# Kernel optimization log

Hardware: AMD Instinct MI355X
Metric: run time of the kernel (lower is better)

## Reference

```python
import jax, jax.numpy as jnp
import numpy as np

KS = 5               # kernel_size per spline dimension
K3 = KS ** 3         # 125 weight matrices per SplineConv
NS = [16384, 4096, 1024, 256, 64]  # nodes per hierarchy level
DEG = 8


def spline_basis(pseudo):
    """Degree-1 open B-spline basis for 3D pseudo-coords in [0,1].
    Returns basis [E,8] and weight indices [E,8] into the K3 weights."""
    v = pseudo * (KS - 1)
    bot = jnp.minimum(jnp.floor(v), KS - 2)
    frac = v - bot                                  # [E,3]
    bot = bot.astype(jnp.int32)
    bits = jnp.array([[(s >> d) & 1 for d in range(3)] for s in range(8)], jnp.int32)  # [8,3]
    f = frac[:, None, :]                            # [E,1,3]
    basis = jnp.prod(jnp.where(bits[None] == 1, f, 1.0 - f), axis=-1)   # [E,8]
    strides = jnp.array([1, KS, KS * KS], jnp.int32)
    widx = jnp.sum((bot[:, None, :] + bits[None]) * strides, axis=-1)   # [E,8]
    return basis, widx


def spline_conv(x, src, dst, basis, widx, W, root, bias, n):
    """out_j = (1/deg_j) * sum_{i->j} sum_s B_s(u_ij) x_i W_{k(s)} + x_j root + bias.
    Accumulate basis-weighted source features into per-(node, weight-index)
    buckets, then one dense einsum with the 125 kernel weights."""
    in_c = x.shape[1]
    contrib = basis[..., None] * x[src][:, None, :]          # [E,8,in]
    flat = (dst[:, None] * K3 + widx).reshape(-1)            # [E*8]
    acc = jnp.zeros((n * K3, in_c), x.dtype).at[flat].add(contrib.reshape(-1, in_c))
    out = jnp.einsum('nki,kio->no', acc.reshape(n, K3, in_c), W)
    deg = jnp.zeros((n,), x.dtype).at[dst].add(1.0)
    return out / jnp.maximum(deg, 1.0)[:, None] + x @ root + bias


def setup_inputs() -> dict:
    rng = np.random.default_rng(0)
    inp = {}
    inp['x'] = jnp.asarray(rng.standard_normal((NS[0], 1)), jnp.float32)
    for l in range(4):
        e = NS[l] * DEG
        inp[f'src{l}'] = jnp.asarray(rng.integers(0, NS[l], e), jnp.int32)
        inp[f'dst{l}'] = jnp.asarray(rng.integers(0, NS[l], e), jnp.int32)
        inp[f'pseudo{l}'] = jnp.asarray(rng.random((e, 3)), jnp.float32)
        cl = np.arange(NS[l]) % NS[l + 1]  # guarantees every voxel cluster non-empty
        rng.shuffle(cl)
        inp[f'cluster{l}'] = jnp.asarray(cl, jnp.int32)
    chans = [(1, 32), (32, 32), (32, 64), (64, 64), (64, 64), (64, 64), (64, 64), (64, 64)]
    names = ['1', '12', '2', '3', '4', '5', '6', '7']
    for nm, (ci, co) in zip(names, chans):
        inp[f'W{nm}'] = jnp.asarray(rng.standard_normal((K3, ci, co)) / np.sqrt(8.0 * ci), jnp.float32)
        inp[f'R{nm}'] = jnp.asarray(rng.standard_normal((ci, co)) / np.sqrt(ci), jnp.float32)
        inp[f'B{nm}'] = jnp.zeros((co,), jnp.float32)
    inp['fc1_w'] = jnp.asarray(rng.standard_normal((64, 64)) / 8.0, jnp.float32)
    inp['fc1_b'] = jnp.zeros((64,), jnp.float32)
    inp['fc2_w'] = jnp.asarray(rng.standard_normal((64, 10)) / 8.0, jnp.float32)
    inp['fc2_b'] = jnp.zeros((10,), jnp.float32)
    return inp


def reference(x, pseudo0, pseudo1, pseudo2, pseudo3,
              src0, dst0, src1, dst1, src2, dst2, src3, dst3,
              cluster0, cluster1, cluster2, cluster3,
              W1, R1, B1, W12, R12, B12, W2, R2, B2, W3, R3, B3,
              W4, R4, B4, W5, R5, B5, W6, R6, B6, W7, R7, B7,
              fc1_w, fc1_b, fc2_w, fc2_b):
    elu = jax.nn.elu
    # level 0
    b, wi = spline_basis(pseudo0)
    h = elu(spline_conv(x, src0, dst0, b, wi, W1, R1, B1, NS[0]))
    h = elu(spline_conv(h, src0, dst0, b, wi, W12, R12, B12, NS[0]))
    h = jax.ops.segment_max(h, cluster0, num_segments=NS[1])   # voxel max pool 1
    # level 1
    b, wi = spline_basis(pseudo1)
    h = elu(spline_conv(h, src1, dst1, b, wi, W2, R2, B2, NS[1]))
    h = elu(spline_conv(h, src1, dst1, b, wi, W3, R3, B3, NS[1]))
    h = jax.ops.segment_max(h, cluster1, num_segments=NS[2])   # voxel max pool 2
    # level 2
    b, wi = spline_basis(pseudo2)
    h = elu(spline_conv(h, src2, dst2, b, wi, W4, R4, B4, NS[2]))
    h = elu(spline_conv(h, src2, dst2, b, wi, W5, R5, B5, NS[2]))
    h = jax.ops.segment_max(h, cluster2, num_segments=NS[3])   # voxel max pool 3
    # level 3
    b, wi = spline_basis(pseudo3)
    h = elu(spline_conv(h, src3, dst3, b, wi, W6, R6, B6, NS[3]))
    h = elu(spline_conv(h, src3, dst3, b, wi, W7, R7, B7, NS[3]))
    h = jax.ops.segment_max(h, cluster3, num_segments=NS[4])   # voxel max pool 4
    # readout head (dropout is identity in eval mode)
    g = h.mean(0)[None, :]
    g = g @ fc1_w + fc1_b
    g = g @ fc2_w + fc2_b
    return jax.nn.log_softmax(g, axis=1)
```

## Files before the change

### kernel.cpp

```cpp
#include <hip/hip_runtime.h>
#include <hip/hip_bf16.h>

#define KS 5
#define K3 125

typedef __attribute__((ext_vector_type(8))) short short8;
typedef __attribute__((ext_vector_type(4))) float floatx4;

__device__ inline unsigned enc_f(float f) {
    int b = __float_as_int(f);
    return (b >= 0) ? ((unsigned)b | 0x80000000u) : ~((unsigned)b);
}

__device__ inline unsigned short f2bf(float f) {
    unsigned u = __float_as_uint(f);
    u += 0x7FFFu + ((u >> 16) & 1u);
    return (unsigned short)(u >> 16);
}
__device__ inline float bf2f(unsigned short h) {
    return __uint_as_float((unsigned)h << 16);
}
__device__ inline unsigned pack2bf(float a, float b) {
    return (unsigned)f2bf(a) | ((unsigned)f2bf(b) << 16);
}

__device__ inline void edge_basis(const float* __restrict__ pseudo, int e,
                                  float* bs, int* ks) {
    float fr[3];
    int bot[3];
#pragma unroll
    for (int d = 0; d < 3; ++d) {
        float v = pseudo[e * 3 + d] * (float)(KS - 1);
        float fl = fminf(floorf(v), (float)(KS - 2));
        fr[d] = v - fl;
        bot[d] = (int)fl;
    }
    const int strides[3] = {1, KS, KS * KS};
#pragma unroll
    for (int s = 0; s < 8; ++s) {
        float b = 1.f;
        int w = 0;
#pragma unroll
        for (int d = 0; d < 3; ++d) {
            int bit = (s >> d) & 1;
            b *= bit ? fr[d] : (1.f - fr[d]);
            w += (bot[d] + bit) * strides[d];
        }
        bs[s] = b;
        ks[s] = w;
    }
}

__device__ inline void edge_fracs(const float* __restrict__ pseudo, int e, float* bs) {
    float fr[3];
#pragma unroll
    for (int d = 0; d < 3; ++d) {
        float v = pseudo[e * 3 + d] * (float)(KS - 1);
        float fl = fminf(floorf(v), (float)(KS - 2));
        fr[d] = v - fl;
    }
#pragma unroll
    for (int s = 0; s < 8; ++s) {
        float b = 1.f;
#pragma unroll
        for (int d = 0; d < 3; ++d) b *= ((s >> d) & 1) ? fr[d] : (1.f - fr[d]);
        bs[s] = b;
    }
}

__device__ inline int edge_bucket(const float* __restrict__ pseudo, int e) {
    int kb = 0;
#pragma unroll
    for (int d = 0; d < 3; ++d) {
        float v = pseudo[e * 3 + d] * (float)(KS - 1);
        int fl = (int)fminf(floorf(v), (float)(KS - 2));
        kb += fl << (2 * d);
    }
    return kb;
}

__global__ __launch_bounds__(256) void pre1(
    const float* __restrict__ p0, const float* __restrict__ p1,
    const float* __restrict__ p2, const float* __restrict__ p3,
    const int* __restrict__ d0, const int* __restrict__ d1,
    const int* __restrict__ d2, const int* __restrict__ d3,
    const int* __restrict__ c0, const int* __restrict__ c1,
    const int* __restrict__ c2, const int* __restrict__ c3,
    const float* __restrict__ w12, const float* __restrict__ w2,
    const float* __restrict__ w3, const float* __restrict__ w4,
    const float* __restrict__ w5, const float* __restrict__ w6,
    const float* __restrict__ w7,
    int* __restrict__ hpart, int* __restrict__ degi,
    int* __restrict__ ccnt, int* __restrict__ clist,
    short* __restrict__ Wt) {
    int b = blockIdx.x;
    if (b >= 765) {
        int idx = (b - 765) * 256 + threadIdx.x;
        if (idx >= 2944000) return;
        const float* Wsrc;
        int lgP, lgI, local;
        if (idx < 128000)       { Wsrc = w12; lgP = 10; lgI = 5; local = idx; }
        else if (idx < 384000)  { Wsrc = w2;  lgP = 11; lgI = 5; local = idx - 128000; }
        else if (idx < 896000)  { Wsrc = w3;  lgP = 12; lgI = 6; local = idx - 384000; }
        else if (idx < 1408000) { Wsrc = w4;  lgP = 12; lgI = 6; local = idx - 896000; }
        else if (idx < 1920000) { Wsrc = w5;  lgP = 12; lgI = 6; local = idx - 1408000; }
        else if (idx < 2432000) { Wsrc = w6;  lgP = 12; lgI = 6; local = idx - 1920000; }
        else                    { Wsrc = w7;  lgP = 12; lgI = 6; local = idx - 2432000; }
        int IC = 1 << lgI;
        int OC = 1 << (lgP - lgI);
        int k = local >> lgP;
        int r = local & ((1 << lgP) - 1);
        int o = r >> lgI;
        int i = r & (IC - 1);
        Wt[idx] = (short)f2bf(Wsrc[(size_t)(k * IC + i) * OC + o]);
        return;
    }
    if (b >= 680) {
        int idx = (b - 680) * 256 + threadIdx.x;
        int j, cof, nof;
        const int* cl;
        if (idx < 16384)      { j = idx;         cl = c0; cof = 0;    nof = 0; }
        else if (idx < 20480) { j = idx - 16384; cl = c1; cof = 4096; nof = 16384; }
        else if (idx < 21504) { j = idx - 20480; cl = c2; cof = 5120; nof = 20480; }
        else if (idx < 21760) { j = idx - 21504; cl = c3; cof = 5376; nof = 21504; }
        else return;
        int c = cl[j];
        int slot = atomicAdd(&ccnt[cof + c], 1) & 3;
        clist[nof + c * 4 + slot] = j;
        return;
    }
    int l, lb, E, dof;
    const float* ps;
    const int* ds;
    if (b < 512)      { l = 0; lb = b;       ps = p0; ds = d0; E = 131072; dof = 0; }
    else if (b < 640) { l = 1; lb = b - 512; ps = p1; ds = d1; E = 32768;  dof = 16384; }
    else if (b < 672) { l = 2; lb = b - 640; ps = p2; ds = d2; E = 8192;   dof = 20480; }
    else              { l = 3; lb = b - 672; ps = p3; ds = d3; E = 2048;   dof = 21504; }
    __shared__ int h[64];
    int t = threadIdx.x;
    if (t < 64) h[t] = 0;
    __syncthreads();
    int e = lb * 256 + t;
    if (e < E) {
        atomicAdd(&h[edge_bucket(ps, e)], 1);
        atomicAdd(&degi[dof + ds[e]], 1);
    }
    __syncthreads();
    if (t < 64) hpart[b * 64 + t] = h[t];
}

__global__ __launch_bounds__(1024) void pre2(const int* __restrict__ hpart,
                                             int* __restrict__ bbase,
                                             int* __restrict__ tileOf,
                                             int* __restrict__ pack,
                                             const int* __restrict__ degi,
                                             int* __restrict__ off,
                                             int* __restrict__ cur) {
    int b = blockIdx.x;
    int t = threadIdx.x;
    __shared__ int ls[1024];
    __shared__ int aux[192];
    if (b < 4) {
        const int Nv[4] = {16384, 4096, 1024, 256};
        const int DOFv[4] = {0, 16384, 20480, 21504};
        const int OFFv[4] = {0, 16385, 20482, 21507};
        int l = b;
        int n = Nv[l];
        const int* d = degi + DOFv[l];
        int* o = off + OFFv[l];
        int* c = cur + DOFv[l];
        int per = (n + 1023) >> 10;
        int beg = t * per;
        int end = (beg + per < n) ? beg + per : n;
        int s = 0;
        for (int j = beg; j < end; ++j) s += d[j];
        ls[t] = s;
        __syncthreads();
        for (int dd = 1; dd < 1024; dd <<= 1) {
            int v = (t >= dd) ? ls[t - dd] : 0;
            __syncthreads();
            ls[t] += v;
            __syncthreads();
        }
        int base = (t == 0) ? 0 : ls[t - 1];
        for (int j = beg; j < end; ++j) {
            o[j] = base;
            c[j] = base;
            base += d[j];
        }
        if (t == 1023) o[n] = ls[1023];
    } else {
        const int TBv[4] = {0, 2112, 2688, 2880};
        const int MTv[4] = {2112, 576, 192, 96};
        const int HBv[4] = {0, 512, 640, 672};
        const int NBv[4] = {512, 128, 32, 8};
        int l = b - 4;
        int tileBase = TBv[l];
        int hb = HBv[l], nb = NBv[l];
        int bucket = t & 63, seg = t >> 6;
        int rps = (nb + 15) >> 4;
        int r0 = seg * rps;
        int r1 = r0 + rps;
        if (r1 > nb) r1 = nb;
        int ssum = 0;
        for (int lb = r0; lb < r1; ++lb) ssum += hpart[(hb + lb) * 64 + bucket];
        ls[seg * 64 + bucket] = ssum;
        __syncthreads();
        int pre = 0;
        for (int s2 = 0; s2 < seg; ++s2) pre += ls[s2 * 64 + bucket];
        if (seg == 15) aux[bucket] = pre + ssum;
        __syncthreads();
        if (t < 64) aux[64 + t] = (aux[t] + 63) >> 6;
        __syncthreads();
        for (int d = 1; d < 64; d <<= 1) {
            int v = 0;
            if (t < 64 && t >= d) v = aux[64 + t - d];
            __syncthreads();
            if (t < 64) aux[64 + t] += v;
            __syncthreads();
        }
        if (t < 64) {
            int cnt = aux[t];
            int tiles = (cnt + 63) >> 6;
            int tb = tileBase + aux[64 + t] - tiles;
            int gstart = tb * 64;
            aux[128 + t] = gstart;
            for (int q = 0; q < tiles; ++q) tileOf[tb + q] = t;
            for (int idx = gstart + cnt; idx < (tb + tiles) * 64; ++idx) pack[idx] = -1;
            if (t == 63) {
                for (int q = tileBase + aux[64 + 63]; q < tileBase + MTv[l]; ++q)
                    tileOf[q] = -1;
            }
        }
        __syncthreads();
        int run = aux[128 + bucket] + pre;
        for (int lb = r0; lb < r1; ++lb) {
            bbase[(hb + lb) * 64 + bucket] = run;
            run += hpart[(hb + lb) * 64 + bucket];
        }
    }
}

__global__ __launch_bounds__(256) void scatter_pos_all(
    const float* __restrict__ p0, const float* __restrict__ p1,
    const float* __restrict__ p2, const float* __restrict__ p3,
    const int* __restrict__ d0, const int* __restrict__ d1,
    const int* __restrict__ d2, const int* __restrict__ d3,
    const int* __restrict__ bbase, int* __restrict__ cur,
    int* __restrict__ pack, int* __restrict__ posArr,
    int* __restrict__ esrt) {
    int b = blockIdx.x;
    int l, lb, E, dof, eof_;
    const float* ps;
    const int* ds;
    if (b < 512)      { l = 0; lb = b;       ps = p0; ds = d0; E = 131072; dof = 0;     eof_ = 0; }
    else if (b < 640) { l = 1; lb = b - 512; ps = p1; ds = d1; E = 32768;  dof = 16384; eof_ = 131072; }
    else if (b < 672) { l = 2; lb = b - 640; ps = p2; ds = d2; E = 8192;   dof = 20480; eof_ = 163840; }
    else              { l = 3; lb = b - 672; ps = p3; ds = d3; E = 2048;   dof = 21504; eof_ = 172032; }
    __shared__ int h[64], lbk[64], gb[64], sh[64];
    __shared__ int sp[256];
    __shared__ unsigned char skk[256];
    int t = threadIdx.x;
    int e = lb * 256 + t;
    int kb = -1;
    if (t < 64) {
        h[t] = 0;
        gb[t] = bbase[b * 64 + t];
    }
    __syncthreads();
    if (e < E) {
        kb = edge_bucket(ps, e);
        atomicAdd(&h[kb], 1);
        int p = atomicAdd(&cur[dof + ds[e]], 1);
        posArr[eof_ + e] = p;
        if (l == 0 && p >= 0 && p < 131072) esrt[p] = e;
    }
    __syncthreads();
    if (t < 64) sh[t] = h[t];
    __syncthreads();
    for (int d = 1; d < 64; d <<= 1) {
        int v = (t < 64 && t >= d) ? sh[t - d] : 0;
        __syncthreads();
        if (t < 64) sh[t] += v;
        __syncthreads();
    }
    if (t < 64) {
        lbk[t] = sh[t] - h[t];
        h[t] = 0;
    }
    __syncthreads();
    if (kb >= 0) {
        int ppos = lbk[kb] + atomicAdd(&h[kb], 1);
        sp[ppos] = e;
        skk[ppos] = (unsigned char)kb;
    }
    __syncthreads();
    int Pb = E - lb * 256;
    if (Pb > 256) Pb = 256;
    if (t < Pb) {
        int k = skk[t];
        pack[gb[k] + (t - lbk[k])] = sp[t];
    }
}

__global__ __launch_bounds__(256) void conv1_fin(
    const float* __restrict__ x, const int* __restrict__ src,
    const float* __restrict__ pseudo, const int* __restrict__ esrt,
    const int* __restrict__ off, const float* __restrict__ W,
    const float* __restrict__ R, const float* __restrict__ B,
    float* __restrict__ out, int n, int Emax) {
    const int lane = threadIdx.x & 63;
    const int wid = threadIdx.x >> 6;
    const int sub = lane >> 5;
    const int o = lane & 31;
    int j = (blockIdx.x * 4 + wid) * 2 + sub;
    if (j >= n) return;
    int b0 = off[j], b1 = off[j + 1];
    if (b0 < 0) b0 = 0;
    if (b1 > Emax) b1 = Emax;
    float acc = 0.f;
    for (int r = b0; r < b1; ++r) {
        int e = esrt[r];
        float bs[8];
        int ks[8];
        edge_basis(pseudo, e, bs, ks);
        float w = 0.f;
#pragma unroll
        for (int s = 0; s < 8; ++s) w = fmaf(bs[s], W[ks[s] * 32 + o], w);
        acc = fmaf(w, x[src[e]], acc);
    }
    float d = fmaxf((float)(b1 - b0), 1.f);
    float v = acc / d + x[j] * R[o] + B[o];
    out[(size_t)j * 32 + o] = (v > 0.f) ? v : expm1f(v);
}

template <int IN_C, int OUT_C>
__global__ __launch_bounds__(256, 4) void mfma_conv(
    const float* __restrict__ x, const int* __restrict__ src,
    const float* __restrict__ pseudo, const int* __restrict__ pack,
    const int* __restrict__ tileOf, const int* __restrict__ pos,
    const short* __restrict__ Wt, unsigned short* __restrict__ y, int tileBase,
    int Emax) {
    constexpr int PH = (IN_C == 64) ? 2 : 1;
    constexpr int SPP = 8 / PH;
    constexpr int KPH = SPP * IN_C;
    constexpr int KP = KPH + 8;
    constexpr int NT = OUT_C / 16;
    constexpr int IP = IN_C / 4;
    __shared__ short As[64 * KP];
    __shared__ int posL[64];
    const int tid = threadIdx.x;
    int t = tileBase + blockIdx.x;
    int kb = tileOf[t];
    if (kb < 0 || kb >= 64) return;
    kb = __builtin_amdgcn_readfirstlane(kb);
    const int kbase = (kb & 3) + 5 * ((kb >> 2) & 3) + 25 * ((kb >> 4) & 3);
    const int eLoc = tid >> 2, part = tid & 3;
    int e = pack[t * 64 + eLoc];
    if (e >= Emax) e = -1;
    float bs[8];
    float4 xq[IP / 4];
    if (e >= 0) edge_fracs(pseudo, e, bs);
    else {
#pragma unroll
        for (int s = 0; s < 8; ++s) bs[s] = 0.f;
    }
    if (part == 0) posL[eLoc] = (e >= 0) ? pos[e] : -1;
#pragma unroll
    for (int g = 0; g < IP / 4; ++g)
        xq[g] = (e >= 0)
                    ? *(const float4*)(x + (size_t)src[e] * IN_C + part * IP + g * 4)
                    : make_float4(0.f, 0.f, 0.f, 0.f);
    const int wave = tid >> 6, lane = tid & 63;
    const int quad = lane >> 4, lm = lane & 15;
    floatx4 acc[NT];
#pragma unroll
    for (int nt = 0; nt < NT; ++nt) acc[nt] = (floatx4){0.f, 0.f, 0.f, 0.f};
    const short* myrow = &As[(wave * 16 + lm) * KP];
#pragma unroll
    for (int ph = 0; ph < PH; ++ph) {
        if (ph) __syncthreads();
#pragma unroll
        for (int s2 = 0; s2 < SPP; ++s2) {
            const float b = bs[ph * SPP + s2];
            short* rowp = &As[eLoc * KP + s2 * IN_C + part * IP];
#pragma unroll
            for (int g = 0; g < IP / 4; ++g) {
                unsigned lo = pack2bf(b * xq[g].x, b * xq[g].y);
                unsigned hi = pack2bf(b * xq[g].z, b * xq[g].w);
                *(uint2*)(rowp + 4 * g) = make_uint2(lo, hi);
            }
        }
        __syncthreads();
#pragma unroll
        for (int kstep = 0; kstep < KPH / 32; ++kstep) {
            const int kg = kstep * 32;
            const int s2 = kg / IN_C;
            const int i0 = kg % IN_C;
            const int s = ph * SPP + s2;
            const int ks = kbase + (s & 1) + 5 * ((s >> 1) & 1) + 25 * ((s >> 2) & 1);
            short8 a = *(const short8*)&myrow[kg + quad * 8];
#pragma unroll
            for (int nt = 0; nt < NT; ++nt) {
                const short* bp =
                    Wt + ((size_t)ks * OUT_C + nt * 16 + lm) * IN_C + i0 + quad * 8;
                short8 bfr = *(const short8*)bp;
                acc[nt] = __builtin_amdgcn_mfma_f32_16x16x32_bf16(a, bfr, acc[nt], 0, 0, 0);
            }
        }
    }
#pragma unroll
    for (int nt = 0; nt < NT; ++nt) {
#pragma unroll
        for (int r = 0; r < 4; ++r) {
            int row = wave * 16 + quad * 4 + r;
            int p = posL[row];
            if (p >= 0 && p < Emax) y[(size_t)p * OUT_C + nt * 16 + lm] = f2bf(acc[nt][r]);
        }
    }
}

template <int OUT_C>
__device__ inline float csr_sum(const int* __restrict__ off,
                                const unsigned short* __restrict__ y, int j, int o,
                                float& dcount) {
    int b0 = off[j], b1 = off[j + 1];
    if (b0 < 0) b0 = 0;
    if (b1 < b0) b1 = b0;
    dcount = fmaxf((float)(b1 - b0), 1.f);
    float s0 = 0.f, s1 = 0.f, s2 = 0.f, s3 = 0.f;
    int r = b0;
    for (; r + 4 <= b1; r += 4) {
        s0 += bf2f(y[(size_t)(r + 0) * OUT_C + o]);
        s1 += bf2f(y[(size_t)(r + 1) * OUT_C + o]);
        s2 += bf2f(y[(size_t)(r + 2) * OUT_C + o]);
        s3 += bf2f(y[(size_t)(r + 3) * OUT_C + o]);
    }
    for (; r < b1; ++r) s0 += bf2f(y[(size_t)r * OUT_C + o]);
    return (s0 + s1) + (s2 + s3);
}

template <int IN_C, int OUT_C>
__global__ __launch_bounds__(256) void fin_gather_k(
    const float* __restrict__ xin, const float* __restrict__ R,
    const float* __restrict__ B, const int* __restrict__ off,
    const unsigned short* __restrict__ y, float* __restrict__ out, int n) {
    const int lane = threadIdx.x & 63;
    const int wid = threadIdx.x >> 6;
    constexpr int EPW = 64 / OUT_C;
    const int sub = (EPW == 2) ? (lane >> 5) : 0;
    const int o = lane & (OUT_C - 1);
    int j = (blockIdx.x * (blockDim.x >> 6) + wid) * EPW + sub;
    if (j >= n) return;
    float xv = (o < IN_C) ? xin[j * IN_C + o] : 0.f;
    float acc = B[o];
#pragma unroll 4
    for (int i = 0; i < IN_C; ++i) {
        float xi = __shfl(xv, i, OUT_C);
        acc = fmaf(xi, R[i * OUT_C + o], acc);
    }
    float d;
    float s = csr_sum<OUT_C>(off, y, j, o, d);
    float v = s / d + acc;
    out[j * OUT_C + o] = (v > 0.f) ? v : expm1f(v);
}

template <int IN_C, int OUT_C>
__global__ __launch_bounds__(256) void fin_pool_k(
    const float* __restrict__ xin, const float* __restrict__ R,
    const float* __restrict__ B, const int* __restrict__ off,
    const unsigned short* __restrict__ y, const int* __restrict__ clist,
    float* __restrict__ out, int nsrc) {
    constexpr int CPB = 256 / (4 * OUT_C);
    const int t = threadIdx.x;
    const int o = t & (OUT_C - 1);
    const int mem = (t / OUT_C) & 3;
    const int g = t / (4 * OUT_C);
    const int c = blockIdx.x * CPB + g;
    int j = clist[c * 4 + mem];
    if (j < 0) j = 0;
    if (j >= nsrc) j = nsrc - 1;
    float xv = (o < IN_C) ? xin[(size_t)j * IN_C + o] : 0.f;
    float acc = B[o];
#pragma unroll 4
    for (int i = 0; i < IN_C; ++i) {
        float xi = __shfl(xv, i, OUT_C);
        acc = fmaf(xi, R[i * OUT_C + o], acc);
    }
    float d;
    float s = csr_sum<OUT_C>(off, y, j, o, d);
    float v = s / d + acc;
    v = (v > 0.f) ? v : expm1f(v);
    __shared__ float sh[256];
    sh[t] = v;
    __syncthreads();
    if (mem == 0) {
        const float* base = &sh[g * 4 * OUT_C];
        float r01 = fmaxf(base[o], base[OUT_C + o]);
        float r23 = fmaxf(base[2 * OUT_C + o], base[3 * OUT_C + o]);
        out[(size_t)c * OUT_C + o] = fmaxf(r01, r23);
    }
}

__global__ __launch_bounds__(256) void conv1_fused(const float* __restrict__ x,
                                                   const int* __restrict__ src,
                                                   const int* __restrict__ dst,
                                                   const float* __restrict__ pseudo,
                                                   const float* __restrict__ W,
                                                   float* __restrict__ out, int E) {
    const int lane = threadIdx.x & 63;
    const int wid = threadIdx.x >> 6;
    const int sub = lane >> 5;
    const int o = lane & 31;
    int e = (blockIdx.x * 4 + wid) * 2 + sub;
    if (e >= E) return;
    float bs[8];
    int ks[8];
    edge_basis(pseudo, e, bs, ks);
    float acc = 0.f;
#pragma unroll
    for (int s = 0; s < 8; ++s) acc = fmaf(bs[s], W[ks[s] * 32 + o], acc);
    atomicAdd(&out[(size_t)dst[e] * 32 + o], acc * x[src[e]]);
}

template <int IN_C, int OUT_C>
__global__ __launch_bounds__(256) void conv_edges_inline(
    const float* __restrict__ x, const int* __restrict__ src,
    const int* __restrict__ dst, const float* __restrict__ pseudo,
    const float* __restrict__ W, float* __restrict__ out, int E) {
    const int lane = threadIdx.x & 63;
    const int wid = threadIdx.x >> 6;
    constexpr int EPW = 64 / OUT_C;
    const int sub = (EPW == 2) ? (lane >> 5) : 0;
    const int o = lane & (OUT_C - 1);
    long e = (long)(blockIdx.x * (blockDim.x >> 6) + wid) * EPW + sub;
    if (e >= E) return;
    float bs[8];
    int ks[8];
    edge_basis(pseudo, e, bs, ks);
    const int s_ = src[e];
    const int d_ = dst[e];
    float xv = (o < IN_C) ? x[s_ * IN_C + o] : 0.f;
    float acc = 0.f;
#pragma unroll
    for (int s = 0; s < 8; ++s) {
        const float b = bs[s];
        const float* Wk = W + (long)ks[s] * IN_C * OUT_C;
#pragma unroll 4
        for (int i = 0; i < IN_C; ++i) {
            float xi = __shfl(xv, i, OUT_C);
            acc = fmaf(b * xi, Wk[i * OUT_C + o], acc);
        }
    }
    atomicAdd(&out[(long)d_ * OUT_C + o], acc);
}

__global__ void deg_kernel(const int* __restrict__ dst, float* __restrict__ deg, int E) {
    int e = blockIdx.x * blockDim.x + threadIdx.x;
    if (e >= E) return;
    atomicAdd(&deg[dst[e]], 1.0f);
}

template <int IN_C, int OUT_C>
__global__ __launch_bounds__(256) void finalize_k(
    const float* __restrict__ xin, const float* __restrict__ R,
    const float* __restrict__ B, const float* __restrict__ deg,
    float* __restrict__ out, int n) {
    const int lane = threadIdx.x & 63;
    const int wid = threadIdx.x >> 6;
    constexpr int EPW = 64 / OUT_C;
    const int sub = (EPW == 2) ? (lane >> 5) : 0;
    const int o = lane & (OUT_C - 1);
    int j = (blockIdx.x * (blockDim.x >> 6) + wid) * EPW + sub;
    if (j >= n) return;
    float xv = (o < IN_C) ? xin[j * IN_C + o] : 0.f;
    float acc = B[o];
#pragma unroll 4
    for (int i = 0; i < IN_C; ++i) {
        float xi = __shfl(xv, i, OUT_C);
        acc = fmaf(xi, R[i * OUT_C + o], acc);
    }
    float d = fmaxf(deg[j], 1.f);
    float v = out[j * OUT_C + o] / d + acc;
    out[j * OUT_C + o] = (v > 0.f) ? v : expm1f(v);
}

__global__ void pool_scatter(const float* __restrict__ h, const int* __restrict__ cluster,
                             unsigned* __restrict__ pool, int n, int logC) {
    int idx = blockIdx.x * blockDim.x + threadIdx.x;
    if (idx >= (n << logC)) return;
    int j = idx >> logC;
    int c = idx & ((1 << logC) - 1);
    atomicMax(&pool[(cluster[j] << logC) + c], enc_f(h[idx]));
}

__global__ void pool_decode(const unsigned* __restrict__ pool, float* __restrict__ out, int total) {
    int idx = blockIdx.x * blockDim.x + threadIdx.x;
    if (idx >= total) return;
    unsigned u = pool[idx];
    int b = (u & 0x80000000u) ? (int)(u & 0x7FFFFFFFu) : (int)(~u);
    out[idx] = __int_as_float(b);
}

__global__ void head_kernel(const float* __restrict__ h, const float* __restrict__ fc1w,
                            const float* __restrict__ fc1b, const float* __restrict__ fc2w,
                            const float* __restrict__ fc2b, float* __restrict__ out) {
    __shared__ float m[64], t[64], u[10];
    int lane = threadIdx.x;
    float s = 0.f;
    for (int j = 0; j < 64; ++j) s += h[j * 64 + lane];
    m[lane] = s * (1.f / 64.f);
    __syncthreads();
    float a = fc1b[lane];
    for (int i = 0; i < 64; ++i) a = fmaf(m[i], fc1w[i * 64 + lane], a);
    t[lane] = a;
    __syncthreads();
    if (lane < 10) {
        float b = fc2b[lane];
        for (int i = 0; i < 64; ++i) b = fmaf(t[i], fc2w[i * 10 + lane], b);
        u[lane] = b;
    }
    __syncthreads();
    if (lane < 10) {
        float mx = u[0];
        for (int i = 1; i < 10; ++i) mx = fmaxf(mx, u[i]);
        float se = 0.f;
        for (int i = 0; i < 10; ++i) se += expf(u[i] - mx);
        out[lane] = u[lane] - mx - logf(se);
    }
}

static inline int cdiv(int a, int b) { return (a + b - 1) / b; }

extern "C" void kernel_launch(void* const* d_in, const int* in_sizes, int n_in,
                              void* d_out, int out_size, void* d_ws, size_t ws_size,
                              hipStream_t stream) {
    const float* x = (const float*)d_in[0];
    const int* src[4] = {(const int*)d_in[1], (const int*)d_in[5], (const int*)d_in[9], (const int*)d_in[13]};
    const int* dst[4] = {(const int*)d_in[2], (const int*)d_in[6], (const int*)d_in[10], (const int*)d_in[14]};
    const float* pseudo[4] = {(const float*)d_in[3], (const float*)d_in[7], (const float*)d_in[11], (const float*)d_in[15]};
    const int* cluster[4] = {(const int*)d_in[4], (const int*)d_in[8], (const int*)d_in[12], (const int*)d_in[16]};
    const float* Wp[8], *Rp[8], *Bp[8];
    for (int l = 0; l < 8; ++l) {
        Wp[l] = (const float*)d_in[17 + 3 * l];
        Rp[l] = (const float*)d_in[18 + 3 * l];
        Bp[l] = (const float*)d_in[19 + 3 * l];
    }
    const float* fc1w = (const float*)d_in[41];
    const float* fc1b = (const float*)d_in[42];
    const float* fc2w = (const float*)d_in[43];
    const float* fc2b = (const float*)d_in[44];
    float* outp = (float*)d_out;

    const int NS[5] = {16384, 4096, 1024, 256, 64};
    const int ES[4] = {16384 * 8, 4096 * 8, 1024 * 8, 256 * 8};
    const int MT[4] = {2048 + 64, 512 + 64, 128 + 64, 32 + 64};
    const int TB_[4] = {0, 2112, 2112 + 576, 2112 + 576 + 192};
    const int TOT_TILES = 2112 + 576 + 192 + 96;
    const int DTOT = 21760;
    const int OFF2[4] = {0, 16385, 20482, 21507};
    const int OFFTOT = 21764;
    const int EBASE[4] = {0, 131072, 163840, 172032};
    const int ETOT = 174080;
    const int NODE_OFF[4] = {0, 16384, 20480, 21504};
    const int CCTOT = 4096 + 1024 + 256 + 64;
    const int HTOT = 680;
    const int WT_OFF[7] = {0, 128000, 384000, 896000, 1408000, 1920000, 2432000};
    const int WT_TOT = 2944000;

    char* w = (char*)d_ws;
    auto take = [&](size_t bytes) -> char* {
        char* r = w;
        w += (bytes + 255) & ~(size_t)255;
        return r;
    };
    float* bufA = (float*)take((size_t)NS[0] * 64 * 4);
    float* bufB = (float*)take((size_t)NS[0] * 64 * 4);
    unsigned* pool = (unsigned*)take((size_t)NS[1] * 64 * 4);
    char* zbase = w;
    int* ccnt = (int*)take((size_t)CCTOT * 4);
    int* degi = (int*)take((size_t)DTOT * 4);
    size_t zbytes = (size_t)(w - zbase);
    size_t fallbackNeed = (size_t)(w - (char*)d_ws);
    int* tileOf = (int*)take((size_t)TOT_TILES * 4);
    int* hpart = (int*)take((size_t)HTOT * 64 * 4);
    int* bbase = (int*)take((size_t)HTOT * 64 * 4);
    int* pack = (int*)take((size_t)TOT_TILES * 64 * 4);
    int* csr = (int*)take((size_t)OFFTOT * 4);
    int* cur = (int*)take((size_t)DTOT * 4);
    int* posArr = (int*)take((size_t)ETOT * 4);
    int* clist = (int*)take((size_t)DTOT * 4);
    int* esrt = (int*)take((size_t)ES[0] * 4);
    short* Wtb = (short*)take((size_t)WT_TOT * 2);
    unsigned short* y = (unsigned short*)take((size_t)ES[0] * 32 * 2);
    size_t need = (size_t)(w - (char*)d_ws);
    bool fast = ws_size >= need;

    const int TB = 256;

    if (fast) {
        (void)hipMemsetAsync(zbase, 0, zbytes, stream);
        pre1<<<765 + cdiv(WT_TOT, 256), 256, 0, stream>>>(
            pseudo[0], pseudo[1], pseudo[2], pseudo[3],
            dst[0], dst[1], dst[2], dst[3],
            cluster[0], cluster[1], cluster[2], cluster[3],
            Wp[1], Wp[2], Wp[3], Wp[4], Wp[5], Wp[6], Wp[7],
            hpart, degi, ccnt, clist, Wtb);
        pre2<<<8, 1024, 0, stream>>>(hpart, bbase, tileOf, pack, degi, csr, cur);
        scatter_pos_all<<<680, 256, 0, stream>>>(pseudo[0], pseudo[1], pseudo[2], pseudo[3],
                                                 dst[0], dst[1], dst[2], dst[3],
                                                 bbase, cur, pack, posArr, esrt);

        {
            int n = NS[0];
            const int* off = csr + OFF2[0];
            const int* pos = posArr + EBASE[0];
            conv1_fin<<<cdiv(n, 8), TB, 0, stream>>>(x, src[0], pseudo[0], esrt, off,
                                                     Wp[0], Rp[0], Bp[0], bufA, n, ES[0]);
            mfma_conv<32, 32><<<MT[0], TB, 0, stream>>>(
                bufA, src[0], pseudo[0], pack, tileOf, pos, Wtb + WT_OFF[0], y, TB_[0], ES[0]);
            fin_pool_k<32, 32><<<NS[1] / 2, TB, 0, stream>>>(
                bufA, Rp[1], Bp[1], off, y, clist + NODE_OFF[0], bufB, NS[0]);
        }
        {
            int n = NS[1];
            const int* off = csr + OFF2[1];
            const int* pos = posArr + EBASE[1];
            mfma_conv<32, 64><<<MT[1], TB, 0, stream>>>(
                bufB, src[1], pseudo[1], pack, tileOf, pos, Wtb + WT_OFF[1], y, TB_[1], ES[1]);
            fin_gather_k<32, 64><<<cdiv(n, 4), TB, 0, stream>>>(bufB, Rp[2], Bp[2], off, y, bufA, n);
            mfma_conv<64, 64><<<MT[1], TB, 0, stream>>>(
                bufA, src[1], pseudo[1], pack, tileOf, pos, Wtb + WT_OFF[2], y, TB_[1], ES[1]);
            fin_pool_k<64, 64><<<NS[2], TB, 0, stream>>>(
                bufA, Rp[3], Bp[3], off, y, clist + NODE_OFF[1], bufB, NS[1]);
        }
        {
            int n = NS[2];
            const int* off = csr + OFF2[2];
            const int* pos = posArr + EBASE[2];
            mfma_conv<64, 64><<<MT[2], TB, 0, stream>>>(
                bufB, src[2], pseudo[2], pack, tileOf, pos, Wtb + WT_OFF[3], y, TB_[2], ES[2]);
            fin_gather_k<64, 64><<<cdiv(n, 4), TB, 0, stream>>>(bufB, Rp[4], Bp[4], off, y, bufA, n);
            mfma_conv<64, 64><<<MT[2], TB, 0, stream>>>(
                bufA, src[2], pseudo[2], pack, tileOf, pos, Wtb + WT_OFF[4], y, TB_[2], ES[2]);
            fin_pool_k<64, 64><<<NS[3], TB, 0, stream>>>(
                bufA, Rp[5], Bp[5], off, y, clist + NODE_OFF[2], bufB, NS[2]);
        }
        {
            int n = NS[3];
            const int* off = csr + OFF2[3];
            const int* pos = posArr + EBASE[3];
            mfma_conv<64, 64><<<MT[3], TB, 0, stream>>>(
                bufB, src[3], pseudo[3], pack, tileOf, pos, Wtb + WT_OFF[5], y, TB_[3], ES[3]);
            fin_gather_k<64, 64><<<cdiv(n, 4), TB, 0, stream>>>(bufB, Rp[6], Bp[6], off, y, bufA, n);
            mfma_conv<64, 64><<<MT[3], TB, 0, stream>>>(
                bufA, src[3], pseudo[3], pack, tileOf, pos, Wtb + WT_OFF[6], y, TB_[3], ES[3]);
            fin_pool_k<64, 64><<<NS[4], TB, 0, stream>>>(
                bufA, Rp[7], Bp[7], off, y, clist + NODE_OFF[3], bufB, NS[3]);
        }
        head_kernel<<<1, 64, 0, stream>>>(bufB, fc1w, fc1b, fc2w, fc2b, outp);
    } else if (ws_size >= fallbackNeed) {
        float* h0 = bufA;
        float* h1 = bufB;
        float* deg = (float*)degi;
        for (int l = 0; l < 4; ++l) {
            int E = ES[l], n = NS[l];
            (void)hipMemsetAsync(deg, 0, n * 4, stream);
            deg_kernel<<<cdiv(E, TB), TB, 0, stream>>>(dst[l], deg, E);
            for (int cc = 0; cc < 2; ++cc) {
                int li = (l == 0) ? cc : 2 * l + cc;
                if (l == 0 && cc == 0) {
                    (void)hipMemsetAsync(h0, 0, (size_t)n * 32 * 4, stream);
                    conv1_fused<<<cdiv(E, 8), TB, 0, stream>>>(x, src[0], dst[0], pseudo[0], Wp[0], h0, E);
                    finalize_k<1, 32><<<cdiv(n, 8), TB, 0, stream>>>(x, Rp[0], Bp[0], deg, h0, n);
                } else {
                    int ic = (l == 0) ? 32 : ((l == 1 && cc == 0) ? 32 : 64);
                    int oc = (l == 0) ? 32 : 64;
                    (void)hipMemsetAsync(h1, 0, (size_t)n * oc * 4, stream);
                    if (ic == 32 && oc == 32) {
                        conv_edges_inline<32, 32><<<cdiv(E, 8), TB, 0, stream>>>(h0, src[l], dst[l], pseudo[l], Wp[li], h1, E);
                        finalize_k<32, 32><<<cdiv(n, 8), TB, 0, stream>>>(h0, Rp[li], Bp[li], deg, h1, n);
                    } else if (ic == 32) {
                        conv_edges_inline<32, 64><<<cdiv(E, 4), TB, 0, stream>>>(h0, src[l], dst[l], pseudo[l], Wp[li], h1, E);
                        finalize_k<32, 64><<<cdiv(n, 4), TB, 0, stream>>>(h0, Rp[li], Bp[li], deg, h1, n);
                    } else {
                        conv_edges_inline<64, 64><<<cdiv(E, 4), TB, 0, stream>>>(h0, src[l], dst[l], pseudo[l], Wp[li], h1, E);
                        finalize_k<64, 64><<<cdiv(n, 4), TB, 0, stream>>>(h0, Rp[li], Bp[li], deg, h1, n);
                    }
                    float* tmp = h0; h0 = h1; h1 = tmp;
                }
            }
            int oc = (l == 0) ? 32 : 64;
            int logC = (l == 0) ? 5 : 6;
            (void)hipMemsetAsync(pool, 0, (size_t)NS[l + 1] * oc * 4, stream);
            pool_scatter<<<cdiv(n * oc, TB), TB, 0, stream>>>(h0, cluster[l], pool, n, logC);
            pool_decode<<<cdiv(NS[l + 1] * oc, TB), TB, 0, stream>>>(pool, h1, NS[l + 1] * oc);
            float* tmp = h0; h0 = h1; h1 = tmp;
        }
        head_kernel<<<1, 64, 0, stream>>>(h0, fc1w, fc1b, fc2w, fc2b, outp);
    }
}
```

Measured before the change: 401.0 us.

## Fuse levels 2-3 and head into one cooperative persistent kernel

Replaces the nine small kernel launches for hierarchy levels 2 and 3 plus the readout head with a single cooperative kernel. The stages are separated by grid-wide syncs instead of kernel boundaries. This targets launch overhead and idle gaps on small workloads, where levels 2 and 3 have few tiles. In exchange it adds grid.sync costs and hardcodes the tile bases and counts (2688, 2880, 192, 96), which makes it brittle to shape changes. It also adds a __syncthreads at the start of each tile.

```diff
diff --git a/kernel.cpp b/kernel.cpp
--- a/kernel.cpp
+++ b/kernel.cpp
@@ -1,5 +1,8 @@
 #include <hip/hip_runtime.h>
 #include <hip/hip_bf16.h>
+#include <hip/hip_cooperative_groups.h>
+
+namespace cg = cooperative_groups;
 
 #define KS 5
 #define K3 125
@@ -335,22 +338,20 @@
 }
 
 template <int IN_C, int OUT_C>
-__global__ __launch_bounds__(256, 4) void mfma_conv(
+__device__ __forceinline__ void mfma_tile_dev(
     const float* __restrict__ x, const int* __restrict__ src,
     const float* __restrict__ pseudo, const int* __restrict__ pack,
     const int* __restrict__ tileOf, const int* __restrict__ pos,
-    const short* __restrict__ Wt, unsigned short* __restrict__ y, int tileBase,
-    int Emax) {
+    const short* __restrict__ Wt, unsigned short* __restrict__ y, int t,
+    int Emax, short* As, int* posL) {
     constexpr int PH = (IN_C == 64) ? 2 : 1;
     constexpr int SPP = 8 / PH;
     constexpr int KPH = SPP * IN_C;
     constexpr int KP = KPH + 8;
     constexpr int NT = OUT_C / 16;
     constexpr int IP = IN_C / 4;
-    __shared__ short As[64 * KP];
-    __shared__ int posL[64];
+    __syncthreads();
     const int tid = threadIdx.x;
-    int t = tileBase + blockIdx.x;
     int kb = tileOf[t];
     if (kb < 0 || kb >= 64) return;
     kb = __builtin_amdgcn_readfirstlane(kb);
@@ -418,6 +419,19 @@
             if (p >= 0 && p < Emax) y[(size_t)p * OUT_C + nt * 16 + lm] = f2bf(acc[nt][r]);
         }
     }
+}
+
+template <int IN_C, int OUT_C>
+__global__ __launch_bounds__(256, 4) void mfma_conv(
+    const float* __restrict__ x, const int* __restrict__ src,
+    const float* __restrict__ pseudo, const int* __restrict__ pack,
+    const int* __restrict__ tileOf, const int* __restrict__ pos,
+    const short* __restrict__ Wt, unsigned short* __restrict__ y, int tileBase,
+    int Emax) {
+    __shared__ short As[64 * 264];
+    __shared__ int posL[64];
+    mfma_tile_dev<IN_C, OUT_C>(x, src, pseudo, pack, tileOf, pos, Wt, y,
+                               tileBase + blockIdx.x, Emax, As, posL);
 }
 
 template <int OUT_C>
@@ -441,16 +455,16 @@
 }
 
 template <int IN_C, int OUT_C>
-__global__ __launch_bounds__(256) void fin_gather_k(
+__device__ __forceinline__ void fin_gather_dev(
     const float* __restrict__ xin, const float* __restrict__ R,
     const float* __restrict__ B, const int* __restrict__ off,
-    const unsigned short* __restrict__ y, float* __restrict__ out, int n) {
+    const unsigned short* __restrict__ y, float* __restrict__ out, int n, int bb) {
     const int lane = threadIdx.x & 63;
     const int wid = threadIdx.x >> 6;
     constexpr int EPW = 64 / OUT_C;
     const int sub = (EPW == 2) ? (lane >> 5) : 0;
     const int o = lane & (OUT_C - 1);
-    int j = (blockIdx.x * (blockDim.x >> 6) + wid) * EPW + sub;
+    int j = (bb * 4 + wid) * EPW + sub;
     if (j >= n) return;
     float xv = (o < IN_C) ? xin[j * IN_C + o] : 0.f;
     float acc = B[o];
@@ -463,6 +477,46 @@
     float s = csr_sum<OUT_C>(off, y, j, o, d);
     float v = s / d + acc;
     out[j * OUT_C + o] = (v > 0.f) ? v : expm1f(v);
+}
+
+template <int IN_C, int OUT_C>
+__global__ __launch_bounds__(256) void fin_gather_k(
+    const float* __restrict__ xin, const float* __restrict__ R,
+    const float* __restrict__ B, const int* __restrict__ off,
+    const unsigned short* __restrict__ y, float* __restrict__ out, int n) {
+    fin_gather_dev<IN_C, OUT_C>(xin, R, B, off, y, out, n, blockIdx.x);
+}
+
+__device__ __forceinline__ void fin_pool64_dev(
+    const float* __restrict__ xin, const float* __restrict__ R,
+    const float* __restrict__ B, const int* __restrict__ off,
+    const unsigned short* __restrict__ y, const int* __restrict__ clist,
+    float* __restrict__ out, int nsrc, int c, float* sh) {
+    const int t = threadIdx.x;
+    const int o = t & 63;
+    const int mem = t >> 6;
+    int j = clist[c * 4 + mem];
+    if (j < 0) j = 0;
+    if (j >= nsrc) j = nsrc - 1;
+    float xv = xin[(size_t)j * 64 + o];
+    float acc = B[o];
+#pragma unroll 4
+    for (int i = 0; i < 64; ++i) {
+        float xi = __shfl(xv, i, 64);
+        acc = fmaf(xi, R[i * 64 + o], acc);
+    }
+    float d;
+    float s = csr_sum<64>(off, y, j, o, d);
+    float v = s / d + acc;
+    v = (v > 0.f) ? v : expm1f(v);
+    sh[t] = v;
+    __syncthreads();
+    if (mem == 0) {
+        float r01 = fmaxf(sh[o], sh[64 + o]);
+        float r23 = fmaxf(sh[128 + o], sh[192 + o]);
+        out[(size_t)c * 64 + o] = fmaxf(r01, r23);
+    }
+    __syncthreads();
 }
 
 template <int IN_C, int OUT_C>
@@ -502,6 +556,98 @@
     }
 }
 
+__device__ __forceinline__ void head_dev(const float* __restrict__ h,
+                                         const float* __restrict__ fc1w,
+                                         const float* __restrict__ fc1b,
+                                         const float* __restrict__ fc2w,
+                                         const float* __restrict__ fc2b,
+                                         float* __restrict__ out, float* sh) {
+    int t = threadIdx.x;
+    if (t < 64) {
+        float s = 0.f;
+        for (int j = 0; j < 64; ++j) s += h[j * 64 + t];
+        sh[t] = s * (1.f / 64.f);
+    }
+    __syncthreads();
+    if (t < 64) {
+        float a = fc1b[t];
+        for (int i = 0; i < 64; ++i) a = fmaf(sh[i], fc1w[i * 64 + t], a);
+        sh[64 + t] = a;
+    }
+    __syncthreads();
+    if (t < 10) {
+        float b = fc2b[t];
+        for (int i = 0; i < 64; ++i) b = fmaf(sh[64 + i], fc2w[i * 10 + t], b);
+        sh[128 + t] = b;
+    }
+    __syncthreads();
+    if (t < 10) {
+        float mx = sh[128];
+        for (int i = 1; i < 10; ++i) mx = fmaxf(mx, sh[128 + i]);
+        float se = 0.f;
+        for (int i = 0; i < 10; ++i) se += expf(sh[128 + i] - mx);
+        out[t] = sh[128 + t] - mx - logf(se);
+    }
+}
+
+__global__ void head_kernel(const float* __restrict__ h, const float* __restrict__ fc1w,
+                            const float* __restrict__ fc1b, const float* __restrict__ fc2w,
+                            const float* __restrict__ fc2b, float* __restrict__ out) {
+    __shared__ float sh[256];
+    head_dev(h, fc1w, fc1b, fc2w, fc2b, out, sh);
+}
+
+struct TailArgs {
+    float* bufA; float* bufB; unsigned short* y;
+    const int* src2; const float* ps2; const int* pos2;
+    const int* src3; const float* ps3; const int* pos3;
+    const int* pack; const int* tileOf;
+    const short* Wt4; const short* Wt5; const short* Wt6; const short* Wt7;
+    const int* off2; const int* off3;
+    const int* cl2; const int* cl3;
+    const float* R4; const float* B4; const float* R5; const float* B5;
+    const float* R6; const float* B6; const float* R7; const float* B7;
+    const float* fc1w; const float* fc1b; const float* fc2w; const float* fc2b;
+    float* outp;
+};
+
+__global__ __launch_bounds__(256) void tail_k(TailArgs a) {
+    __shared__ short As[64 * 264];
+    __shared__ int posL[64];
+    __shared__ float shf[256];
+    cg::grid_group grid = cg::this_grid();
+    for (int tt = blockIdx.x; tt < 192; tt += gridDim.x)
+        mfma_tile_dev<64, 64>(a.bufB, a.src2, a.ps2, a.pack, a.tileOf, a.pos2,
+                              a.Wt4, a.y, 2688 + tt, 8192, As, posL);
+    grid.sync();
+    for (int bb = blockIdx.x; bb < 256; bb += gridDim.x)
+        fin_gather_dev<64, 64>(a.bufB, a.R4, a.B4, a.off2, a.y, a.bufA, 1024, bb);
+    grid.sync();
+    for (int tt = blockIdx.x; tt < 192; tt += gridDim.x)
+        mfma_tile_dev<64, 64>(a.bufA, a.src2, a.ps2, a.pack, a.tileOf, a.pos2,
+                              a.Wt5, a.y, 2688 + tt, 8192, As, posL);
+    grid.sync();
+    for (int c = blockIdx.x; c < 256; c += gridDim.x)
+        fin_pool64_dev(a.bufA, a.R5, a.B5, a.off2, a.y, a.cl2, a.bufB, 1024, c, shf);
+    grid.sync();
+    for (int tt = blockIdx.x; tt < 96; tt += gridDim.x)
+        mfma_tile_dev<64, 64>(a.bufB, a.src3, a.ps3, a.pack, a.tileOf, a.pos3,
+                              a.Wt6, a.y, 2880 + tt, 2048, As, posL);
+    grid.sync();
+    for (int bb = blockIdx.x; bb < 64; bb += gridDim.x)
+        fin_gather_dev<64, 64>(a.bufB, a.R6, a.B6, a.off3, a.y, a.bufA, 256, bb);
+    grid.sync();
+    for (int tt = blockIdx.x; tt < 96; tt += gridDim.x)
+        mfma_tile_dev<64, 64>(a.bufA, a.src3, a.ps3, a.pack, a.tileOf, a.pos3,
+                              a.Wt7, a.y, 2880 + tt, 2048, As, posL);
+    grid.sync();
+    for (int c = blockIdx.x; c < 64; c += gridDim.x)
+        fin_pool64_dev(a.bufA, a.R7, a.B7, a.off3, a.y, a.cl3, a.bufB, 256, c, shf);
+    grid.sync();
+    if (blockIdx.x == 0)
+        head_dev(a.bufB, a.fc1w, a.fc1b, a.fc2w, a.fc2b, a.outp, shf);
+}
+
 __global__ __launch_bounds__(256) void conv1_fused(const float* __restrict__ x,
                                                    const int* __restrict__ src,
                                                    const int* __restrict__ dst,
@@ -600,34 +746,6 @@
     unsigned u = pool[idx];
     int b = (u & 0x80000000u) ? (int)(u & 0x7FFFFFFFu) : (int)(~u);
     out[idx] = __int_as_float(b);
-}
-
-__global__ void head_kernel(const float* __restrict__ h, const float* __restrict__ fc1w,
-                            const float* __restrict__ fc1b, const float* __restrict__ fc2w,
-                            const float* __restrict__ fc2b, float* __restrict__ out) {
-    __shared__ float m[64], t[64], u[10];
-    int lane = threadIdx.x;
-    float s = 0.f;
-    for (int j = 0; j < 64; ++j) s += h[j * 64 + lane];
-    m[lane] = s * (1.f / 64.f);
-    __syncthreads();
-    float a = fc1b[lane];
-    for (int i = 0; i < 64; ++i) a = fmaf(m[i], fc1w[i * 64 + lane], a);
-    t[lane] = a;
-    __syncthreads();
-    if (lane < 10) {
-        float b = fc2b[lane];
-        for (int i = 0; i < 64; ++i) b = fmaf(t[i], fc2w[i * 10 + lane], b);
-        u[lane] = b;
-    }
-    __syncthreads();
-    if (lane < 10) {
-        float mx = u[0];
-        for (int i = 1; i < 10; ++i) mx = fmaxf(mx, u[i]);
-        float se = 0.f;
-        for (int i = 0; i < 10; ++i) se += expf(u[i] - mx);
-        out[lane] = u[lane] - mx - logf(se);
-    }
 }
 
 static inline int cdiv(int a, int b) { return (a + b - 1) / b; }
@@ -735,30 +853,23 @@
                 bufA, Rp[3], Bp[3], off, y, clist + NODE_OFF[1], bufB, NS[1]);
         }
         {
-            int n = NS[2];
-            const int* off = csr + OFF2[2];
-            const int* pos = posArr + EBASE[2];
-            mfma_conv<64, 64><<<MT[2], TB, 0, stream>>>(
-                bufB, src[2], pseudo[2], pack, tileOf, pos, Wtb + WT_OFF[3], y, TB_[2], ES[2]);
-            fin_gather_k<64, 64><<<cdiv(n, 4), TB, 0, stream>>>(bufB, Rp[4], Bp[4], off, y, bufA, n);
-            mfma_conv<64, 64><<<MT[2], TB, 0, stream>>>(
-                bufA, src[2], pseudo[2], pack, tileOf, pos, Wtb + WT_OFF[4], y, TB_[2], ES[2]);
-            fin_pool_k<64, 64><<<NS[3], TB, 0, stream>>>(
-                bufA, Rp[5], Bp[5], off, y, clist + NODE_OFF[2], bufB, NS[2]);
-        }
-        {
-            int n = NS[3];
-            const int* off = csr + OFF2[3];
-            const int* pos = posArr + EBASE[3];
-            mfma_conv<64, 64><<<MT[3], TB, 0, stream>>>(
-                bufB, src[3], pseudo[3], pack, tileOf, pos, Wtb + WT_OFF[5], y, TB_[3], ES[3]);
-            fin_gather_k<64, 64><<<cdiv(n, 4), TB, 0, stream>>>(bufB, Rp[6], Bp[6], off, y, bufA, n);
-            mfma_conv<64, 64><<<MT[3], TB, 0, stream>>>(
-                bufA, src[3], pseudo[3], pack, tileOf, pos, Wtb + WT_OFF[6], y, TB_[3], ES[3]);
-            fin_pool_k<64, 64><<<NS[4], TB, 0, stream>>>(
-                bufA, Rp[7], Bp[7], off, y, clist + NODE_OFF[3], bufB, NS[3]);
-        }
-        head_kernel<<<1, 64, 0, stream>>>(bufB, fc1w, fc1b, fc2w, fc2b, outp);
+            TailArgs ta;
+            ta.bufA = bufA; ta.bufB = bufB; ta.y = y;
+            ta.src2 = src[2]; ta.ps2 = pseudo[2]; ta.pos2 = posArr + EBASE[2];
+            ta.src3 = src[3]; ta.ps3 = pseudo[3]; ta.pos3 = posArr + EBASE[3];
+            ta.pack = pack; ta.tileOf = tileOf;
+            ta.Wt4 = Wtb + WT_OFF[3]; ta.Wt5 = Wtb + WT_OFF[4];
+            ta.Wt6 = Wtb + WT_OFF[5]; ta.Wt7 = Wtb + WT_OFF[6];
+            ta.off2 = csr + OFF2[2]; ta.off3 = csr + OFF2[3];
+            ta.cl2 = clist + NODE_OFF[2]; ta.cl3 = clist + NODE_OFF[3];
+            ta.R4 = Rp[4]; ta.B4 = Bp[4]; ta.R5 = Rp[5]; ta.B5 = Bp[5];
+            ta.R6 = Rp[6]; ta.B6 = Bp[6]; ta.R7 = Rp[7]; ta.B7 = Bp[7];
+            ta.fc1w = fc1w; ta.fc1b = fc1b; ta.fc2w = fc2w; ta.fc2b = fc2b;
+            ta.outp = outp;
+            void* kargs[] = {&ta};
+            (void)hipLaunchCooperativeKernel(reinterpret_cast<void*>(tail_k),
+                                             dim3(192), dim3(256), kargs, 0, stream);
+        }
     } else if (ws_size >= fallbackNeed) {
         float* h0 = bufA;
         float* h1 = bufB;
```

New measurement: 628.9 us. 1.57x slower.

## Transpose weights via shared-memory tiles and split MFMA conv into more phases

Applied to the files above, without the earlier changes.

The weight bf16 conversion in pre1 now processes one 125-slice matrix per block, loading it coalesced into padded LDS and writing it back transposed. This replaces strided global reads, one thread per element, and cuts the block count from about 11500 to 875. Separately, mfma_conv doubles its phase count so each phase stages fewer spline slots in LDS, and launch bounds rise from 4 to 6 blocks per CU. The aim is higher occupancy, at the cost of more phase iterations and syncs, and possible register pressure.

```diff
diff --git a/kernel.cpp b/kernel.cpp
--- a/kernel.cpp
+++ b/kernel.cpp
@@ -93,30 +93,46 @@
     int* __restrict__ hpart, int* __restrict__ degi,
     int* __restrict__ ccnt, int* __restrict__ clist,
     short* __restrict__ Wt) {
+    __shared__ float wls[64 * 65];
+    __shared__ int h[64];
     int b = blockIdx.x;
+    int t = threadIdx.x;
     if (b >= 765) {
-        int idx = (b - 765) * 256 + threadIdx.x;
-        if (idx >= 2944000) return;
-        const float* Wsrc;
-        int lgP, lgI, local;
-        if (idx < 128000)       { Wsrc = w12; lgP = 10; lgI = 5; local = idx; }
-        else if (idx < 384000)  { Wsrc = w2;  lgP = 11; lgI = 5; local = idx - 128000; }
-        else if (idx < 896000)  { Wsrc = w3;  lgP = 12; lgI = 6; local = idx - 384000; }
-        else if (idx < 1408000) { Wsrc = w4;  lgP = 12; lgI = 6; local = idx - 896000; }
-        else if (idx < 1920000) { Wsrc = w5;  lgP = 12; lgI = 6; local = idx - 1408000; }
-        else if (idx < 2432000) { Wsrc = w6;  lgP = 12; lgI = 6; local = idx - 1920000; }
-        else                    { Wsrc = w7;  lgP = 12; lgI = 6; local = idx - 2432000; }
-        int IC = 1 << lgI;
-        int OC = 1 << (lgP - lgI);
-        int k = local >> lgP;
-        int r = local & ((1 << lgP) - 1);
-        int o = r >> lgI;
-        int i = r & (IC - 1);
-        Wt[idx] = (short)f2bf(Wsrc[(size_t)(k * IC + i) * OC + o]);
+        int sl = b - 765;
+        const float* srcp;
+        int IC, OC, lgI, lgO, per;
+        size_t obase;
+        if (sl < 125) {
+            IC = 32; OC = 32; lgI = 5; lgO = 5; per = 1024;
+            srcp = w12 + (size_t)sl * 1024;
+            obase = (size_t)sl * 1024;
+        } else if (sl < 250) {
+            int k = sl - 125;
+            IC = 32; OC = 64; lgI = 5; lgO = 6; per = 2048;
+            srcp = w2 + (size_t)k * 2048;
+            obase = 128000 + (size_t)k * 2048;
+        } else {
+            int q = sl - 250;
+            int ts = q / 125;
+            int k = q - ts * 125;
+            const float* Ws[5] = {w3, w4, w5, w6, w7};
+            IC = 64; OC = 64; lgI = 6; lgO = 6; per = 4096;
+            srcp = Ws[ts] + (size_t)k * 4096;
+            obase = 384000 + (size_t)ts * 512000 + (size_t)k * 4096;
+        }
+        for (int r = t; r < per; r += 256) {
+            int i = r >> lgO, o = r & (OC - 1);
+            wls[i * (OC + 1) + o] = srcp[r];
+        }
+        __syncthreads();
+        for (int j = t; j < per; j += 256) {
+            int o = j >> lgI, i = j & (IC - 1);
+            Wt[obase + j] = (short)f2bf(wls[i * (OC + 1) + o]);
+        }
         return;
     }
     if (b >= 680) {
-        int idx = (b - 680) * 256 + threadIdx.x;
+        int idx = (b - 680) * 256 + t;
         int j, cof, nof;
         const int* cl;
         if (idx < 16384)      { j = idx;         cl = c0; cof = 0;    nof = 0; }
@@ -136,8 +152,6 @@
     else if (b < 640) { l = 1; lb = b - 512; ps = p1; ds = d1; E = 32768;  dof = 16384; }
     else if (b < 672) { l = 2; lb = b - 640; ps = p2; ds = d2; E = 8192;   dof = 20480; }
     else              { l = 3; lb = b - 672; ps = p3; ds = d3; E = 2048;   dof = 21504; }
-    __shared__ int h[64];
-    int t = threadIdx.x;
     if (t < 64) h[t] = 0;
     __syncthreads();
     int e = lb * 256 + t;
@@ -335,13 +349,13 @@
 }
 
 template <int IN_C, int OUT_C>
-__global__ __launch_bounds__(256, 4) void mfma_conv(
+__global__ __launch_bounds__(256, 6) void mfma_conv(
     const float* __restrict__ x, const int* __restrict__ src,
     const float* __restrict__ pseudo, const int* __restrict__ pack,
     const int* __restrict__ tileOf, const int* __restrict__ pos,
     const short* __restrict__ Wt, unsigned short* __restrict__ y, int tileBase,
     int Emax) {
-    constexpr int PH = (IN_C == 64) ? 2 : 1;
+    constexpr int PH = (IN_C == 64) ? 4 : 2;
     constexpr int SPP = 8 / PH;
     constexpr int KPH = SPP * IN_C;
     constexpr int KP = KPH + 8;
@@ -667,6 +681,7 @@
     const int HTOT = 680;
     const int WT_OFF[7] = {0, 128000, 384000, 896000, 1408000, 1920000, 2432000};
     const int WT_TOT = 2944000;
+    const int NSLICE = 875;
 
     char* w = (char*)d_ws;
     auto take = [&](size_t bytes) -> char* {
@@ -700,7 +715,7 @@
 
     if (fast) {
         (void)hipMemsetAsync(zbase, 0, zbytes, stream);
-        pre1<<<765 + cdiv(WT_TOT, 256), 256, 0, stream>>>(
+        pre1<<<765 + NSLICE, 256, 0, stream>>>(
             pseudo[0], pseudo[1], pseudo[2], pseudo[3],
             dst[0], dst[1], dst[2], dst[3],
             cluster[0], cluster[1], cluster[2], cluster[3],
```

After: 403.0 us. About the same (+0.5%).
